# Optimization experiments

Measured on AMD Instinct MI355X. Metric: run time of the kernel, lower is better.

## Reference

```python
import jax, jax.numpy as jnp
import numpy as np

HALF_HIDDEN = 64  # hidden_size // 2


def _lstm_scan(xs, W_ih, W_hh):
    # xs: [T, B, H]; returns final (h, c), each [B, half_hidden]
    B = xs.shape[1]
    h0 = jnp.zeros((B, HALF_HIDDEN), xs.dtype)
    c0 = jnp.zeros((B, HALF_HIDDEN), xs.dtype)

    def step(carry, x_t):
        h, c = carry
        gates = x_t @ W_ih.T + h @ W_hh.T          # [B, 4*hh]
        i_g, f_g, g_g, o_g = jnp.split(gates, 4, axis=1)
        c_new = jax.nn.sigmoid(f_g) * c + jax.nn.sigmoid(i_g) * jnp.tanh(g_g)
        h_new = jax.nn.sigmoid(o_g) * jnp.tanh(c_new)
        return (h_new, c_new), None

    (h, c), _ = jax.lax.scan(step, (h0, c0), xs)
    return h, c


def setup_inputs() -> dict:
    key = jax.random.key(0)
    ks = jax.random.split(key, 8)
    B, T, V, H, HH = 1024, 512, 128, 128, HALF_HIDDEN
    scale = 0.1
    return {
        "x": jax.random.randint(ks[0], (B, T), 0, V, dtype=jnp.int32),
        "lengths": jax.random.randint(ks[1], (B,), 1, T, dtype=jnp.int32),
        "emb": jax.random.normal(ks[2], (V, H), jnp.float32) * scale,
        "W_ih_f": jax.random.normal(ks[3], (4 * HH, H), jnp.float32) * scale,
        "W_hh_f": jax.random.normal(ks[4], (4 * HH, HH), jnp.float32) * scale,
        "W_ih_b": jax.random.normal(ks[5], (4 * HH, H), jnp.float32) * scale,
        "W_hh_b": jax.random.normal(ks[6], (4 * HH, HH), jnp.float32) * scale,
        "W_fc": jax.random.normal(ks[7], (V, H), jnp.float32) * scale,
        "b_fc": jnp.zeros((V,), jnp.float32),
    }


def reference(x, lengths, emb, W_ih_f, W_hh_f, W_ih_b, W_hh_b, W_fc, b_fc):
    # embedding lookup: [B, T, H] -> time-major [T, B, H]
    embedded = emb[x]
    xs = jnp.transpose(embedded, (1, 0, 2))
    h_f, _ = _lstm_scan(xs, W_ih_f, W_hh_f)            # forward direction
    h_b, _ = _lstm_scan(xs[::-1], W_ih_b, W_hh_b)      # backward direction
    hidden_cat = jnp.concatenate([h_f, h_b], axis=1)   # [B, hidden]
    return hidden_cat @ W_fc.T + b_fc                  # [B, vocab]
```

## Files before the change

### kernel.cpp

```cpp
#include <hip/hip_runtime.h>
#include <hip/hip_bf16.h>


#define T_STEPS 512
#define BATCH   1024
#define VOCAB   128
#define HID     128
#define HH      64
#define NG      256
#define MB      4
#define XPAD    8

#define L2E  1.4426950408889634f
#define L2E2 2.8853900817779268f

typedef __attribute__((ext_vector_type(8))) short bf16x8;
typedef __attribute__((ext_vector_type(4))) float f32x4;
typedef unsigned int  u32;
typedef unsigned short u16;

__device__ __forceinline__ float sigmoid_f(float x) {
    return __builtin_amdgcn_rcpf(1.0f + __builtin_amdgcn_exp2f(-x * L2E));
}
__device__ __forceinline__ float tanh_f(float x) {
    return 1.0f - 2.0f * __builtin_amdgcn_rcpf(1.0f + __builtin_amdgcn_exp2f(x * L2E2));
}
__device__ __forceinline__ u16 f2bf_rne(float f) {
    u32 u = __builtin_bit_cast(u32, f);
    u += 0x7FFFu + ((u >> 16) & 1u);
    return (u16)(u >> 16);
}
__device__ __forceinline__ void barrier_lgkm() {
    asm volatile("s_waitcnt lgkmcnt(0)\n\ts_barrier" ::: "memory");
}

__global__ __launch_bounds__(256) void build_tab_kernel(
    const float* __restrict__ emb,
    const float* __restrict__ W_ih_f,
    const float* __restrict__ W_ih_b,
    const float* __restrict__ W_hh_f,
    const float* __restrict__ W_hh_b,
    float* __restrict__ tab3,
    u16*   __restrict__ whh_bf)
{
    int v = blockIdx.x, d = blockIdx.y, tid = threadIdx.x;
    int j = tid >> 2, g = tid & 3;
    int gr = g * HH + j;
    const float* W = d ? W_ih_b : W_ih_f;
    const float4* e4 = (const float4*)(emb + v * HID);
    const float4* w4 = (const float4*)(W + gr * HID);
    float acc = 0.0f;
#pragma unroll
    for (int k = 0; k < HID / 4; ++k) {
        float4 e = e4[k]; float4 w = w4[k];
        acc += e.x * w.x + e.y * w.y + e.z * w.z + e.w * w.w;
    }
    tab3[(d * VOCAB + v) * NG + j * 4 + g] = acc;

    if (tid < 128) {
        const float* Whh = d ? W_hh_b : W_hh_f;
        int idx = v * 128 + tid;
        whh_bf[d * NG * HH + idx] = f2bf_rne(Whh[idx]);
    }
}

__global__ __launch_bounds__(256, 2) void lstm_rec_kernel(
    const int*  __restrict__ x,
    const u16*  __restrict__ whh_bf,
    const float* __restrict__ tab3,
    float* __restrict__ hfin)
{
    __shared__ u32 xs4[T_STEPS + 2 * XPAD][MB];
    __shared__ __align__(16) u16 hbuf[2][MB][72];

    const int tid  = threadIdx.x;
    const int lane = tid & 63;
    const int wave = tid >> 6;
    const int quad = lane >> 4;
    const int m    = lane & 15;
    const int dir    = blockIdx.y;
    const int b_base = blockIdx.x * MB;

    for (int i = tid; i < MB * T_STEPS; i += 256) {
        int bl = i >> 9, t = i & (T_STEPS - 1);
        xs4[XPAD + t][bl] = ((u32)x[(b_base + bl) * T_STEPS + t]) << 10;
    }
    if (tid < MB * XPAD) {
        ((u32*)xs4)[tid] = 0;
        ((u32*)xs4)[(XPAD + T_STEPS) * MB + tid] = 0;
    }
    for (int i = tid; i < 2 * MB * 72 / 2; i += 256)
        ((u32*)hbuf)[i] = 0;

    const u16* WB = whh_bf + dir * NG * HH;
    bf16x8 Bg[4][2];
#pragma unroll
    for (int g = 0; g < 4; ++g)
#pragma unroll
        for (int kc = 0; kc < 2; ++kc)
            Bg[g][kc] = *(const bf16x8*)(WB + (g * HH + wave * 16 + m) * HH
                                            + kc * 32 + quad * 8);

    const char* tabB = (const char*)(tab3 + dir * VOCAB * NG);
    const u32 joff = (u32)(wave * 16 + m) * 16u;
    const int aoff = (m >> 2) * 72 + quad * 8;
    const int woff = quad * 72 + wave * 16 + m;

    const f32x4 z4 = {0.f, 0.f, 0.f, 0.f};
    float cc = 0.f, hcur = 0.f;
    float4 X0, X1;
    u32 vA;

    __syncthreads();

    {
        int ta = XPAD + (dir ? T_STEPS - 1 : 0);
        X0 = *(const float4*)(tabB + xs4[ta][quad] + joff);
        int tb = XPAD + (dir ? T_STEPS - 2 : 1);
        vA = xs4[tb][quad];
    }

    auto stepf = [&](const u16* rh, u16* wh,
                     const float4& Xc, float4& Xn, int s) {
        bf16x8 Ah0 = *(const bf16x8*)(rh + aoff);
        bf16x8 Ah1 = *(const bf16x8*)(rh + aoff + 32);

        Xn = *(const float4*)(tabB + vA + joff);
        {
            int t2 = XPAD + (dir ? (T_STEPS - 3 - s) : (s + 2));
            vA = xs4[t2][quad];
        }

        f32x4 aI = __builtin_amdgcn_mfma_f32_16x16x32_bf16(Ah0, Bg[0][0], z4, 0, 0, 0);
        f32x4 aF = __builtin_amdgcn_mfma_f32_16x16x32_bf16(Ah0, Bg[1][0], z4, 0, 0, 0);
        f32x4 aG = __builtin_amdgcn_mfma_f32_16x16x32_bf16(Ah0, Bg[2][0], z4, 0, 0, 0);
        f32x4 aO = __builtin_amdgcn_mfma_f32_16x16x32_bf16(Ah0, Bg[3][0], z4, 0, 0, 0);
        aI = __builtin_amdgcn_mfma_f32_16x16x32_bf16(Ah1, Bg[0][1], aI, 0, 0, 0);
        aF = __builtin_amdgcn_mfma_f32_16x16x32_bf16(Ah1, Bg[1][1], aF, 0, 0, 0);
        aG = __builtin_amdgcn_mfma_f32_16x16x32_bf16(Ah1, Bg[2][1], aG, 0, 0, 0);
        aO = __builtin_amdgcn_mfma_f32_16x16x32_bf16(Ah1, Bg[3][1], aO, 0, 0, 0);

        float gi = aI[0] + Xc.x;
        float gf = aF[0] + Xc.y;
        float gg = aG[0] + Xc.z;
        float go = aO[0] + Xc.w;

        cc   = sigmoid_f(gf) * cc + sigmoid_f(gi) * tanh_f(gg);
        hcur = sigmoid_f(go) * tanh_f(cc);

        wh[woff] = f2bf_rne(hcur);
    };

    for (int it = 0; it < T_STEPS / 2; ++it) {
        stepf(&hbuf[0][0][0], &hbuf[1][0][0], X0, X1, 2 * it);
        barrier_lgkm();
        stepf(&hbuf[1][0][0], &hbuf[0][0][0], X1, X0, 2 * it + 1);
        barrier_lgkm();
    }

    hfin[(dir * BATCH + b_base + quad) * HH + wave * 16 + m] = hcur;
}

__global__ __launch_bounds__(256) void fc_kernel(
    const float* __restrict__ hfin,
    const float* __restrict__ W_fc,
    const float* __restrict__ b_fc,
    float* __restrict__ out)
{
    __shared__ float wfc[HID * 129];
    __shared__ float hid[8][HID];
    const int tid = threadIdx.x;
    const int b0  = blockIdx.x * 8;

    for (int i = tid; i < HID * HID; i += 256) {
        int r = i >> 7, c = i & 127;
        wfc[r * 129 + c] = W_fc[i];
    }
    for (int i = tid; i < 8 * HID; i += 256) {
        int bb = i >> 7, v = i & 127;
        hid[bb][v] = (v < HH) ? hfin[(0 * BATCH + b0 + bb) * HH + v]
                              : hfin[(1 * BATCH + b0 + bb) * HH + (v - HH)];
    }
    __syncthreads();

    const int v  = tid & 127;
    const int bs = (tid >> 7) * 4;
    const float bias = b_fc[v];
    const float* wrow = wfc + v * 129;
#pragma unroll
    for (int r = 0; r < 4; ++r) {
        const float* h = hid[bs + r];
        float acc = bias;
#pragma unroll
        for (int k = 0; k < HID; k += 4) {
            acc += wrow[k]     * h[k]     + wrow[k + 1] * h[k + 1]
                 + wrow[k + 2] * h[k + 2] + wrow[k + 3] * h[k + 3];
        }
        out[(b0 + bs + r) * HID + v] = acc;
    }
}

extern "C" void kernel_launch(void* const* d_in, const int* in_sizes, int n_in,
                              void* d_out, int out_size, void* d_ws, size_t ws_size,
                              hipStream_t stream) {
    const int*   x      = (const int*)d_in[0];
    const float* emb    = (const float*)d_in[2];
    const float* W_ih_f = (const float*)d_in[3];
    const float* W_hh_f = (const float*)d_in[4];
    const float* W_ih_b = (const float*)d_in[5];
    const float* W_hh_b = (const float*)d_in[6];
    const float* W_fc   = (const float*)d_in[7];
    const float* b_fc   = (const float*)d_in[8];
    float* out = (float*)d_out;

    float* tab3   = (float*)d_ws;
    u16*   whh_bf = (u16*)(tab3 + 2 * VOCAB * NG);
    float* hfin   = (float*)(whh_bf + 2 * NG * HH);

    build_tab_kernel<<<dim3(VOCAB, 2), 256, 0, stream>>>(
        emb, W_ih_f, W_ih_b, W_hh_f, W_hh_b, tab3, whh_bf);
    lstm_rec_kernel<<<dim3(BATCH / MB, 2), 256, 0, stream>>>(x, whh_bf, tab3, hfin);
    fc_kernel<<<dim3(BATCH / 8), 256, 0, stream>>>(hfin, W_fc, b_fc, out);
}
```

Before: 216.1 us.

## Process two independent 4-row batch groups per block to interleave recurrences

Each block now carries two independent 4-batch LSTM chains (8 rows), issuing both sets of MFMAs and gate math within one barrier step. Independent work now sits between each step's dependent chain of MFMA, transcendental ops and LDS write, and the grid halves to 256 blocks (512 with both directions). Token indices are stored time-reversed per direction and read four at a time as int4 from LDS, and the loop is unrolled by eight. The risk is lower occupancy (launch bounds 1) and fewer blocks, so fewer CUs may be busy.

```diff
diff --git a/kernel.cpp b/kernel.cpp
--- a/kernel.cpp
+++ b/kernel.cpp
@@ -8,8 +8,7 @@
 #define HID     128
 #define HH      64
 #define NG      256
-#define MB      4
-#define XPAD    8
+#define XPITCH  520
 
 #define L2E  1.4426950408889634f
 #define L2E2 2.8853900817779268f
@@ -64,14 +63,14 @@
     }
 }
 
-__global__ __launch_bounds__(256, 2) void lstm_rec_kernel(
+__global__ __launch_bounds__(256, 1) void lstm_rec_kernel(
     const int*  __restrict__ x,
     const u16*  __restrict__ whh_bf,
     const float* __restrict__ tab3,
     float* __restrict__ hfin)
 {
-    __shared__ u32 xs4[T_STEPS + 2 * XPAD][MB];
-    __shared__ __align__(16) u16 hbuf[2][MB][72];
+    __shared__ u32 xsT[8][XPITCH];
+    __shared__ __align__(16) u16 hbuf[2][2][4][80];
 
     const int tid  = threadIdx.x;
     const int lane = tid & 63;
@@ -79,17 +78,16 @@
     const int quad = lane >> 4;
     const int m    = lane & 15;
     const int dir    = blockIdx.y;
-    const int b_base = blockIdx.x * MB;
-
-    for (int i = tid; i < MB * T_STEPS; i += 256) {
+    const int b_base = blockIdx.x * 8;
+
+    for (int i = tid; i < 8 * T_STEPS; i += 256) {
         int bl = i >> 9, t = i & (T_STEPS - 1);
-        xs4[XPAD + t][bl] = ((u32)x[(b_base + bl) * T_STEPS + t]) << 10;
-    }
-    if (tid < MB * XPAD) {
-        ((u32*)xs4)[tid] = 0;
-        ((u32*)xs4)[(XPAD + T_STEPS) * MB + tid] = 0;
-    }
-    for (int i = tid; i < 2 * MB * 72 / 2; i += 256)
+        int ts = dir ? (T_STEPS - 1 - t) : t;
+        xsT[bl][ts] = ((u32)x[(b_base + bl) * T_STEPS + t]) << 10;
+    }
+    if (tid < 64)
+        xsT[tid >> 3][T_STEPS + (tid & 7)] = 0;
+    for (int i = tid; i < (int)(sizeof(hbuf) / 4); i += 256)
         ((u32*)hbuf)[i] = 0;
 
     const u16* WB = whh_bf + dir * NG * HH;
@@ -101,64 +99,99 @@
             Bg[g][kc] = *(const bf16x8*)(WB + (g * HH + wave * 16 + m) * HH
                                             + kc * 32 + quad * 8);
 
-    const char* tabB = (const char*)(tab3 + dir * VOCAB * NG);
+    const char* tabB = (const char*)tab3 + (size_t)dir * VOCAB * NG * 4;
     const u32 joff = (u32)(wave * 16 + m) * 16u;
-    const int aoff = (m >> 2) * 72 + quad * 8;
-    const int woff = quad * 72 + wave * 16 + m;
+    const int aoff = (m >> 2) * 80 + quad * 8;
+    const int woff = quad * 80 + wave * 16 + m;
 
     const f32x4 z4 = {0.f, 0.f, 0.f, 0.f};
-    float cc = 0.f, hcur = 0.f;
-    float4 X0, X1;
-    u32 vA;
+    float cc0 = 0.f, h0 = 0.f;
+    float cc1 = 0.f, h1 = 0.f;
 
     __syncthreads();
 
+    int4 q0A = *(const int4*)&xsT[quad][0];
+    int4 q0B = *(const int4*)&xsT[quad][4];
+    int4 q1A = *(const int4*)&xsT[4 + quad][0];
+    int4 q1B = *(const int4*)&xsT[4 + quad][4];
+
+    float4 XA0 = *(const float4*)(tabB + (u32)q0A.x + joff);
+    float4 XA1 = *(const float4*)(tabB + (u32)q1A.x + joff);
+    float4 XB0, XB1;
+
+    auto stepf = [&](int p, const float4 Xc0, const float4 Xc1,
+                     float4& Xn0, float4& Xn1, u32 e0, u32 e1) {
+        const u16* r0 = &hbuf[0][p][0][0];
+        const u16* r1 = &hbuf[1][p][0][0];
+        u16* w0 = &hbuf[0][p ^ 1][0][0];
+        u16* w1 = &hbuf[1][p ^ 1][0][0];
+        bf16x8 A00 = *(const bf16x8*)(r0 + aoff);
+        bf16x8 A01 = *(const bf16x8*)(r0 + aoff + 32);
+        bf16x8 A10 = *(const bf16x8*)(r1 + aoff);
+        bf16x8 A11 = *(const bf16x8*)(r1 + aoff + 32);
+
+        Xn0 = *(const float4*)(tabB + e0 + joff);
+        Xn1 = *(const float4*)(tabB + e1 + joff);
+
+        f32x4 aI = __builtin_amdgcn_mfma_f32_16x16x32_bf16(A00, Bg[0][0], z4, 0, 0, 0);
+        f32x4 aF = __builtin_amdgcn_mfma_f32_16x16x32_bf16(A00, Bg[1][0], z4, 0, 0, 0);
+        f32x4 aG = __builtin_amdgcn_mfma_f32_16x16x32_bf16(A00, Bg[2][0], z4, 0, 0, 0);
+        f32x4 aO = __builtin_amdgcn_mfma_f32_16x16x32_bf16(A00, Bg[3][0], z4, 0, 0, 0);
+        aI = __builtin_amdgcn_mfma_f32_16x16x32_bf16(A01, Bg[0][1], aI, 0, 0, 0);
+        aF = __builtin_amdgcn_mfma_f32_16x16x32_bf16(A01, Bg[1][1], aF, 0, 0, 0);
+        aG = __builtin_amdgcn_mfma_f32_16x16x32_bf16(A01, Bg[2][1], aG, 0, 0, 0);
+        aO = __builtin_amdgcn_mfma_f32_16x16x32_bf16(A01, Bg[3][1], aO, 0, 0, 0);
+
+        float gi0 = aI[0] + Xc0.x;
+        float gf0 = aF[0] + Xc0.y;
+        float gg0 = aG[0] + Xc0.z;
+        float go0 = aO[0] + Xc0.w;
+
+        f32x4 bI = __builtin_amdgcn_mfma_f32_16x16x32_bf16(A10, Bg[0][0], z4, 0, 0, 0);
+        f32x4 bF = __builtin_amdgcn_mfma_f32_16x16x32_bf16(A10, Bg[1][0], z4, 0, 0, 0);
+        f32x4 bG = __builtin_amdgcn_mfma_f32_16x16x32_bf16(A10, Bg[2][0], z4, 0, 0, 0);
+        f32x4 bO = __builtin_amdgcn_mfma_f32_16x16x32_bf16(A10, Bg[3][0], z4, 0, 0, 0);
+        bI = __builtin_amdgcn_mfma_f32_16x16x32_bf16(A11, Bg[0][1], bI, 0, 0, 0);
+        bF = __builtin_amdgcn_mfma_f32_16x16x32_bf16(A11, Bg[1][1], bF, 0, 0, 0);
+        bG = __builtin_amdgcn_mfma_f32_16x16x32_bf16(A11, Bg[2][1], bG, 0, 0, 0);
+        bO = __builtin_amdgcn_mfma_f32_16x16x32_bf16(A11, Bg[3][1], bO, 0, 0, 0);
+
+        float gi1 = bI[0] + Xc1.x;
+        float gf1 = bF[0] + Xc1.y;
+        float gg1 = bG[0] + Xc1.z;
+        float go1 = bO[0] + Xc1.w;
+
+        cc0 = sigmoid_f(gf0) * cc0 + sigmoid_f(gi0) * tanh_f(gg0);
+        h0  = sigmoid_f(go0) * tanh_f(cc0);
+        cc1 = sigmoid_f(gf1) * cc1 + sigmoid_f(gi1) * tanh_f(gg1);
+        h1  = sigmoid_f(go1) * tanh_f(cc1);
+
+        w0[woff] = f2bf_rne(h0);
+        w1[woff] = f2bf_rne(h1);
+
+        barrier_lgkm();
+    };
+
+    for (int kk = 0; kk < T_STEPS / 8; ++kk) {
+        stepf(0, XA0, XA1, XB0, XB1, (u32)q0A.y, (u32)q1A.y);
+        stepf(1, XB0, XB1, XA0, XA1, (u32)q0A.z, (u32)q1A.z);
+        stepf(0, XA0, XA1, XB0, XB1, (u32)q0A.w, (u32)q1A.w);
+        q0A = *(const int4*)&xsT[quad][8 * kk + 8];
+        q1A = *(const int4*)&xsT[4 + quad][8 * kk + 8];
+        stepf(1, XB0, XB1, XA0, XA1, (u32)q0B.x, (u32)q1B.x);
+        stepf(0, XA0, XA1, XB0, XB1, (u32)q0B.y, (u32)q1B.y);
+        stepf(1, XB0, XB1, XA0, XA1, (u32)q0B.z, (u32)q1B.z);
+        stepf(0, XA0, XA1, XB0, XB1, (u32)q0B.w, (u32)q1B.w);
+        q0B = *(const int4*)&xsT[quad][8 * kk + 12];
+        q1B = *(const int4*)&xsT[4 + quad][8 * kk + 12];
+        stepf(1, XB0, XB1, XA0, XA1, (u32)q0A.x, (u32)q1A.x);
+    }
+
     {
-        int ta = XPAD + (dir ? T_STEPS - 1 : 0);
-        X0 = *(const float4*)(tabB + xs4[ta][quad] + joff);
-        int tb = XPAD + (dir ? T_STEPS - 2 : 1);
-        vA = xs4[tb][quad];
-    }
-
-    auto stepf = [&](const u16* rh, u16* wh,
-                     const float4& Xc, float4& Xn, int s) {
-        bf16x8 Ah0 = *(const bf16x8*)(rh + aoff);
-        bf16x8 Ah1 = *(const bf16x8*)(rh + aoff + 32);
-
-        Xn = *(const float4*)(tabB + vA + joff);
-        {
-            int t2 = XPAD + (dir ? (T_STEPS - 3 - s) : (s + 2));
-            vA = xs4[t2][quad];
-        }
-
-        f32x4 aI = __builtin_amdgcn_mfma_f32_16x16x32_bf16(Ah0, Bg[0][0], z4, 0, 0, 0);
-        f32x4 aF = __builtin_amdgcn_mfma_f32_16x16x32_bf16(Ah0, Bg[1][0], z4, 0, 0, 0);
-        f32x4 aG = __builtin_amdgcn_mfma_f32_16x16x32_bf16(Ah0, Bg[2][0], z4, 0, 0, 0);
-        f32x4 aO = __builtin_amdgcn_mfma_f32_16x16x32_bf16(Ah0, Bg[3][0], z4, 0, 0, 0);
-        aI = __builtin_amdgcn_mfma_f32_16x16x32_bf16(Ah1, Bg[0][1], aI, 0, 0, 0);
-        aF = __builtin_amdgcn_mfma_f32_16x16x32_bf16(Ah1, Bg[1][1], aF, 0, 0, 0);
-        aG = __builtin_amdgcn_mfma_f32_16x16x32_bf16(Ah1, Bg[2][1], aG, 0, 0, 0);
-        aO = __builtin_amdgcn_mfma_f32_16x16x32_bf16(Ah1, Bg[3][1], aO, 0, 0, 0);
-
-        float gi = aI[0] + Xc.x;
-        float gf = aF[0] + Xc.y;
-        float gg = aG[0] + Xc.z;
-        float go = aO[0] + Xc.w;
-
-        cc   = sigmoid_f(gf) * cc + sigmoid_f(gi) * tanh_f(gg);
-        hcur = sigmoid_f(go) * tanh_f(cc);
-
-        wh[woff] = f2bf_rne(hcur);
-    };
-
-    for (int it = 0; it < T_STEPS / 2; ++it) {
-        stepf(&hbuf[0][0][0], &hbuf[1][0][0], X0, X1, 2 * it);
-        barrier_lgkm();
-        stepf(&hbuf[1][0][0], &hbuf[0][0][0], X1, X0, 2 * it + 1);
-        barrier_lgkm();
-    }
-
-    hfin[(dir * BATCH + b_base + quad) * HH + wave * 16 + m] = hcur;
+        int j = wave * 16 + m;
+        hfin[(dir * BATCH + b_base + quad) * HH + j]     = h0;
+        hfin[(dir * BATCH + b_base + 4 + quad) * HH + j] = h1;
+    }
 }
 
 __global__ __launch_bounds__(256) void fc_kernel(
@@ -219,6 +252,6 @@
 
     build_tab_kernel<<<dim3(VOCAB, 2), 256, 0, stream>>>(
         emb, W_ih_f, W_ih_b, W_hh_f, W_hh_b, tab3, whh_bf);
-    lstm_rec_kernel<<<dim3(BATCH / MB, 2), 256, 0, stream>>>(x, whh_bf, tab3, hfin);
+    lstm_rec_kernel<<<dim3(BATCH / 8, 2), 256, 0, stream>>>(x, whh_bf, tab3, hfin);
     fc_kernel<<<dim3(BATCH / 8), 256, 0, stream>>>(hfin, W_fc, b_fc, out);
 }
```

Measured after the change: 266.3 us. +23.2%, slower.

## Vectorize token index prefetch, pad h buffer, hardware bf16 convert, set wave priority

Applied to the files above, without the earlier changes.

Stores token offsets per batch row in time-ordered layout, reversed for the backward direction, so each wave fetches four upcoming indices with one 128-bit LDS read instead of a scalar LDS read every step. The loop is unrolled by eight with the barrier moved inside the step. The h buffer pitch changes from 72 to 80 to alter the LDS bank mapping, and the bf16 conversion uses the v_cvt_pk_bf16_f32 instruction. s_setprio raises wave priority around the MFMA section. The aim is to shorten the serial per-step latency chain of the recurrence, at the cost of more code and register pressure.

```diff
diff --git a/kernel.cpp b/kernel.cpp
--- a/kernel.cpp
+++ b/kernel.cpp
@@ -9,7 +9,7 @@
 #define HH      64
 #define NG      256
 #define MB      4
-#define XPAD    8
+#define XPITCH  520
 
 #define L2E  1.4426950408889634f
 #define L2E2 2.8853900817779268f
@@ -70,8 +70,8 @@
     const float* __restrict__ tab3,
     float* __restrict__ hfin)
 {
-    __shared__ u32 xs4[T_STEPS + 2 * XPAD][MB];
-    __shared__ __align__(16) u16 hbuf[2][MB][72];
+    __shared__ __align__(16) u32 xsT[MB][XPITCH];
+    __shared__ __align__(16) u16 hbuf[2][MB][80];
 
     const int tid  = threadIdx.x;
     const int lane = tid & 63;
@@ -83,13 +83,12 @@
 
     for (int i = tid; i < MB * T_STEPS; i += 256) {
         int bl = i >> 9, t = i & (T_STEPS - 1);
-        xs4[XPAD + t][bl] = ((u32)x[(b_base + bl) * T_STEPS + t]) << 10;
-    }
-    if (tid < MB * XPAD) {
-        ((u32*)xs4)[tid] = 0;
-        ((u32*)xs4)[(XPAD + T_STEPS) * MB + tid] = 0;
-    }
-    for (int i = tid; i < 2 * MB * 72 / 2; i += 256)
+        int ts = dir ? (T_STEPS - 1 - t) : t;
+        xsT[bl][ts] = ((u32)x[(b_base + bl) * T_STEPS + t]) << 10;
+    }
+    if (tid < MB * 8)
+        xsT[tid >> 3][T_STEPS + (tid & 7)] = 0;
+    for (int i = tid; i < (int)(sizeof(hbuf) / 4); i += 256)
         ((u32*)hbuf)[i] = 0;
 
     const u16* WB = whh_bf + dir * NG * HH;
@@ -101,35 +100,29 @@
             Bg[g][kc] = *(const bf16x8*)(WB + (g * HH + wave * 16 + m) * HH
                                             + kc * 32 + quad * 8);
 
-    const char* tabB = (const char*)(tab3 + dir * VOCAB * NG);
+    const char* tabB = (const char*)tab3 + (size_t)dir * VOCAB * NG * 4;
     const u32 joff = (u32)(wave * 16 + m) * 16u;
-    const int aoff = (m >> 2) * 72 + quad * 8;
-    const int woff = quad * 72 + wave * 16 + m;
+    const int aoff = (m >> 2) * 80 + quad * 8;
+    const int woff = quad * 80 + wave * 16 + m;
 
     const f32x4 z4 = {0.f, 0.f, 0.f, 0.f};
     float cc = 0.f, hcur = 0.f;
-    float4 X0, X1;
-    u32 vA;
 
     __syncthreads();
 
-    {
-        int ta = XPAD + (dir ? T_STEPS - 1 : 0);
-        X0 = *(const float4*)(tabB + xs4[ta][quad] + joff);
-        int tb = XPAD + (dir ? T_STEPS - 2 : 1);
-        vA = xs4[tb][quad];
-    }
-
-    auto stepf = [&](const u16* rh, u16* wh,
-                     const float4& Xc, float4& Xn, int s) {
+    int4 qA = *(const int4*)&xsT[quad][0];
+    int4 qB = *(const int4*)&xsT[quad][4];
+    float4 X0 = *(const float4*)(tabB + (u32)qA.x + joff);
+    float4 X1;
+
+    auto stepf = [&](int p, const float4 Xc, float4& Xn, u32 e) {
+        __builtin_amdgcn_s_setprio(1);
+        const u16* rh = &hbuf[p][0][0];
+        u16* wh = &hbuf[p ^ 1][0][0];
         bf16x8 Ah0 = *(const bf16x8*)(rh + aoff);
         bf16x8 Ah1 = *(const bf16x8*)(rh + aoff + 32);
 
-        Xn = *(const float4*)(tabB + vA + joff);
-        {
-            int t2 = XPAD + (dir ? (T_STEPS - 3 - s) : (s + 2));
-            vA = xs4[t2][quad];
-        }
+        Xn = *(const float4*)(tabB + e + joff);
 
         f32x4 aI = __builtin_amdgcn_mfma_f32_16x16x32_bf16(Ah0, Bg[0][0], z4, 0, 0, 0);
         f32x4 aF = __builtin_amdgcn_mfma_f32_16x16x32_bf16(Ah0, Bg[1][0], z4, 0, 0, 0);
@@ -144,18 +137,29 @@
         float gf = aF[0] + Xc.y;
         float gg = aG[0] + Xc.z;
         float go = aO[0] + Xc.w;
+        __builtin_amdgcn_s_setprio(0);
 
         cc   = sigmoid_f(gf) * cc + sigmoid_f(gi) * tanh_f(gg);
         hcur = sigmoid_f(go) * tanh_f(cc);
 
-        wh[woff] = f2bf_rne(hcur);
+        u32 hb;
+        asm("v_cvt_pk_bf16_f32 %0, %1, %2" : "=v"(hb) : "v"(hcur), "v"(hcur));
+        wh[woff] = (u16)hb;
+
+        barrier_lgkm();
     };
 
-    for (int it = 0; it < T_STEPS / 2; ++it) {
-        stepf(&hbuf[0][0][0], &hbuf[1][0][0], X0, X1, 2 * it);
-        barrier_lgkm();
-        stepf(&hbuf[1][0][0], &hbuf[0][0][0], X1, X0, 2 * it + 1);
-        barrier_lgkm();
+    for (int kk = 0; kk < T_STEPS / 8; ++kk) {
+        stepf(0, X0, X1, (u32)qA.y);
+        stepf(1, X1, X0, (u32)qA.z);
+        stepf(0, X0, X1, (u32)qA.w);
+        qA = *(const int4*)&xsT[quad][8 * kk + 8];
+        stepf(1, X1, X0, (u32)qB.x);
+        stepf(0, X0, X1, (u32)qB.y);
+        stepf(1, X1, X0, (u32)qB.z);
+        stepf(0, X0, X1, (u32)qB.w);
+        qB = *(const int4*)&xsT[quad][8 * kk + 12];
+        stepf(1, X1, X0, (u32)qA.x);
     }
 
     hfin[(dir * BATCH + b_base + quad) * HH + wave * 16 + m] = hcur;
```

Result: no change. 214.4 us (-0.8%).
